# Performance work log

Hardware: AMD Instinct MI355X
Metric: run time of the kernel (lower is better)

The kernel has to match this reference:

```python
import jax, jax.numpy as jnp
import numpy as np

TEMPERATURE = 0.5
NUM_NEG_CANDIDATES = 8
HARD_NEG_K = 3


def setup_inputs() -> dict:
    key = jax.random.key(0)
    k1, k2 = jax.random.split(key)
    features = jax.random.normal(k1, (8192, 512), dtype=jnp.float32)
    labels = jax.random.randint(k2, (8192,), 0, 64, dtype=jnp.int64)
    return {"features": features, "labels": labels}


def reference(features, labels):
    B = features.shape[0]
    labels = labels.reshape(-1)
    # L2-normalize rows (torch F.normalize, eps=1e-12)
    f = features / jnp.maximum(jnp.linalg.norm(features, axis=1, keepdims=True), 1e-12)

    same = labels[:, None] == labels[None, :]          # [B, B]
    eye = jnp.eye(B, dtype=bool)
    neg_inf = jnp.float32(-jnp.inf)

    # Deterministic replacement for torch's randint/randperm sampling:
    # Gumbel-max = uniform sampling of one positive; Gumbel-top-m = sampling
    # m negatives without replacement.
    kp, kn = jax.random.split(jax.random.key(42))
    g_pos = jax.random.gumbel(kp, (B, B), dtype=jnp.float32)
    g_neg = jax.random.gumbel(kn, (B, B), dtype=jnp.float32)

    pos_mask = same & ~eye
    pos_j = jnp.argmax(jnp.where(pos_mask, g_pos, neg_inf), axis=1)   # [B]

    _, neg_idx = jax.lax.top_k(jnp.where(~same, g_neg, neg_inf), NUM_NEG_CANDIDATES)  # [B, m]

    cand = f[neg_idx]                                  # [B, m, D]
    neg_sims = jnp.einsum('bd,bmd->bm', f, cand)       # [B, m]
    hard_sims, _ = jax.lax.top_k(neg_sims, HARD_NEG_K)  # [B, k] hardest negatives

    pos_logit = jnp.sum(f * f[pos_j], axis=1) / TEMPERATURE          # [B]
    logits = jnp.concatenate([pos_logit[:, None], hard_sims / TEMPERATURE], axis=1)  # [B, 1+k]
    # cross-entropy with target index 0
    loss = jax.nn.logsumexp(logits, axis=1) - logits[:, 0]
    return jnp.mean(loss)
```

## Files before the change

### kernel.cpp

```cpp
#include <hip/hip_runtime.h>
#include <hip/hip_bf16.h>
#include <stdint.h>

#define BB 8192
#define DD 512
#define NNEG 8
#define CAP 256

#define VTHI 4273471488u

__host__ __device__ __forceinline__ uint32_t rotl32(uint32_t x, int r) {
#if defined(__HIP_DEVICE_COMPILE__)
  return __builtin_amdgcn_alignbit(x, x, 32 - r);
#else
  return (x << r) | (x >> (32 - r));
#endif
}

#define TF_RND(x0, x1, R) { x0 += x1; x1 = rotl32(x1, R); x1 ^= x0; }

__host__ __device__ __forceinline__ void threefry2x32(uint32_t k0, uint32_t k1,
                                                      uint32_t x0, uint32_t x1,
                                                      uint32_t& o0, uint32_t& o1) {
  uint32_t ks2 = k0 ^ k1 ^ 0x1BD11BDAu;
  x0 += k0; x1 += k1;
  TF_RND(x0, x1, 13) TF_RND(x0, x1, 15) TF_RND(x0, x1, 26) TF_RND(x0, x1, 6)
  x0 += k1; x1 += ks2 + 1u;
  TF_RND(x0, x1, 17) TF_RND(x0, x1, 29) TF_RND(x0, x1, 16) TF_RND(x0, x1, 24)
  x0 += ks2; x1 += k0 + 2u;
  TF_RND(x0, x1, 13) TF_RND(x0, x1, 15) TF_RND(x0, x1, 26) TF_RND(x0, x1, 6)
  x0 += k0; x1 += k1 + 3u;
  TF_RND(x0, x1, 17) TF_RND(x0, x1, 29) TF_RND(x0, x1, 16) TF_RND(x0, x1, 24)
  x0 += k1; x1 += ks2 + 4u;
  TF_RND(x0, x1, 13) TF_RND(x0, x1, 15) TF_RND(x0, x1, 26) TF_RND(x0, x1, 6)
  x0 += ks2; x1 += k0 + 5u;
  o0 = x0; o1 = x1;
}

__device__ __forceinline__ void tf_uniform(uint32_t k0, uint32_t k1, uint32_t x1pk,
                                           uint32_t& o0, uint32_t& o1) {
  uint32_t ks2 = k0 ^ k1 ^ 0x1BD11BDAu;
  uint32_t x0 = k0, x1 = x1pk;
  TF_RND(x0, x1, 13) TF_RND(x0, x1, 15) TF_RND(x0, x1, 26) TF_RND(x0, x1, 6)
  x0 += k1; x1 += ks2 + 1u;
  TF_RND(x0, x1, 17) TF_RND(x0, x1, 29) TF_RND(x0, x1, 16) TF_RND(x0, x1, 24)
  x0 += ks2; x1 += k0 + 2u;
  TF_RND(x0, x1, 13) TF_RND(x0, x1, 15) TF_RND(x0, x1, 26) TF_RND(x0, x1, 6)
  x0 += k0; x1 += k1 + 3u;
  TF_RND(x0, x1, 17) TF_RND(x0, x1, 29) TF_RND(x0, x1, 16) TF_RND(x0, x1, 24)
  x0 += k1; x1 += ks2 + 4u;
  TF_RND(x0, x1, 13) TF_RND(x0, x1, 15) TF_RND(x0, x1, 26) TF_RND(x0, x1, 6)
  x0 += ks2; x1 += k0 + 5u;
  o0 = x0; o1 = x1;
}

#define RND4(R) { TF_RND(x0a, x1a, R) TF_RND(x0b, x1b, R) TF_RND(x0c, x1c, R) TF_RND(x0d, x1d, R) }
#define INJ4(A, B) { uint32_t _b = (B); \
  x0a += (A); x1a += _b; x0b += (A); x1b += _b; x0c += (A); x1c += _b; x0d += (A); x1d += _b; }

__device__ __forceinline__ void tf_uniform4(uint32_t k0, uint32_t k1, uint32_t ctr,
                                            uint32_t bits[4]) {
  uint32_t ks2 = k0 ^ k1 ^ 0x1BD11BDAu;
  uint32_t x0a = k0, x1a = ctr;
  uint32_t x0b = k0, x1b = ctr + 64u;
  uint32_t x0c = k0, x1c = ctr + 128u;
  uint32_t x0d = k0, x1d = ctr + 192u;
  RND4(13) RND4(15) RND4(26) RND4(6)
  INJ4(k1, ks2 + 1u)
  RND4(17) RND4(29) RND4(16) RND4(24)
  INJ4(ks2, k0 + 2u)
  RND4(13) RND4(15) RND4(26) RND4(6)
  INJ4(k0, k1 + 3u)
  RND4(17) RND4(29) RND4(16) RND4(24)
  INJ4(k1, ks2 + 4u)
  RND4(13) RND4(15) RND4(26) RND4(6)
  INJ4(ks2, k0 + 5u)
  bits[0] = x0a ^ x1a; bits[1] = x0b ^ x1b; bits[2] = x0c ^ x1c; bits[3] = x0d ^ x1d;
}

__device__ __forceinline__ unsigned long long u64max(unsigned long long a, unsigned long long b) {
  return a > b ? a : b;
}
#define CE_DESC(m, x, y) { if (m[x] < m[y]) { unsigned long long _t = m[x]; m[x] = m[y]; m[y] = _t; } }
#define TOP8_INSERT(top, key) \
  if ((key) > top[7]) { \
    top[7] = (key); \
    _Pragma("unroll") \
    for (int s = 7; s > 0; --s) { \
      if (top[s] > top[s - 1]) { \
        unsigned long long _tt = top[s - 1]; top[s - 1] = top[s]; top[s] = _tt; \
      } \
    } \
  }

__device__ __forceinline__ void wave_merge_top8(unsigned long long top[8]) {
  #pragma unroll
  for (int d = 1; d < 64; d <<= 1) {
    unsigned long long o[8];
    #pragma unroll
    for (int r = 0; r < 8; ++r) o[r] = __shfl_xor(top[r], d, 64);
    unsigned long long m[8];
    #pragma unroll
    for (int r = 0; r < 8; ++r) m[r] = u64max(top[r], o[7 - r]);
    CE_DESC(m, 0, 4) CE_DESC(m, 1, 5) CE_DESC(m, 2, 6) CE_DESC(m, 3, 7)
    CE_DESC(m, 0, 2) CE_DESC(m, 1, 3) CE_DESC(m, 4, 6) CE_DESC(m, 5, 7)
    CE_DESC(m, 0, 1) CE_DESC(m, 2, 3) CE_DESC(m, 4, 5) CE_DESC(m, 6, 7)
    #pragma unroll
    for (int r = 0; r < 8; ++r) top[r] = m[r];
  }
}

__global__ __launch_bounds__(256) void prep_kernel(const float* __restrict__ feat,
                                                   const int* __restrict__ labels,
                                                   float* __restrict__ inv_norm,
                                                   uint16_t* __restrict__ lists,
                                                   int* __restrict__ offs) {
  if (blockIdx.x == 0) {
    __shared__ uint32_t hist[64];
    __shared__ uint32_t base[64];
    int t = threadIdx.x;
    if (t < 64) hist[t] = 0u;
    __syncthreads();
    for (int e = t; e < BB; e += 256) atomicAdd(&hist[labels[e] & 63], 1u);
    __syncthreads();
    if (t == 0) {
      uint32_t s = 0;
      for (int l = 0; l < 64; ++l) { base[l] = s; offs[l] = (int)s; s += hist[l]; }
      offs[64] = (int)s;
    }
    __syncthreads();
    for (int e = t; e < BB; e += 256) {
      uint32_t p = atomicAdd(&base[labels[e] & 63], 1u);
      lists[p] = (uint16_t)e;
    }
  } else {
    int wave = threadIdx.x >> 6, lane = threadIdx.x & 63;
    int row = (blockIdx.x - 1) * 4 + wave;
    const float4* fr = (const float4*)(feat + (size_t)row * DD);
    float4 a = fr[lane], b = fr[lane + 64];
    float s = a.x * a.x + a.y * a.y + a.z * a.z + a.w * a.w
            + b.x * b.x + b.y * b.y + b.z * b.z + b.w * b.w;
    #pragma unroll
    for (int d = 1; d < 64; d <<= 1) s += __shfl_xor(s, d, 64);
    if (lane == 0) inv_norm[row] = 1.0f / fmaxf(sqrtf(s), 1e-12f);
  }
}

__global__ __launch_bounds__(256) void scan_kernel(const int* __restrict__ labels,
                                                   const uint16_t* __restrict__ lists,
                                                   const int* __restrict__ offs,
                                                   uint32_t kp0, uint32_t kp1,
                                                   uint32_t kn0, uint32_t kn1,
                                                   int* __restrict__ pos_j,
                                                   int* __restrict__ neg_idx) {
  __shared__ uint2 buf[4][CAP];
  int wave = threadIdx.x >> 6, lane = threadIdx.x & 63;
  int i = blockIdx.x * 4 + wave;
  int li = labels[i];
  uint32_t rowbase = (uint32_t)i * (uint32_t)BB;
  uint32_t count = 0;

  uint32_t cb = rowbase + kn1 + (uint32_t)lane;
  for (int it = 0; it < BB / 256; ++it) {
    uint32_t bits[4];
    tf_uniform4(kn0, kn1, cb + (uint32_t)(it * 256), bits);
    #pragma unroll
    for (int c = 0; c < 4; ++c) {
      bool cand = bits[c] >= VTHI;
      unsigned long long m = __ballot(cand);
      if (m) {
        if (cand) {
          int ofs = __builtin_amdgcn_mbcnt_hi((uint32_t)(m >> 32),
                     __builtin_amdgcn_mbcnt_lo((uint32_t)m, 0));
          uint32_t p = count + (uint32_t)ofs;
          if (p < CAP) {
            uint2 e; e.x = bits[c]; e.y = (uint32_t)(it * 256 + c * 64 + lane);
            buf[wave][p] = e;
          }
        }
        count += (uint32_t)__popcll(m);
      }
    }
  }

  unsigned long long best = 0ull;
  int beg = offs[li], end = offs[li + 1];
  for (int t = beg + lane; t < end; t += 64) {
    int j = lists[t];
    if (j != i) {
      uint32_t o0, o1;
      tf_uniform(kp0, kp1, rowbase + kp1 + (uint32_t)j, o0, o1);
      unsigned long long key =
          (((unsigned long long)((o0 ^ o1) >> 9) << 13) | (unsigned)(8191 - j)) + 1ull;
      best = u64max(best, key);
    }
  }
  #pragma unroll
  for (int d = 1; d < 64; d <<= 1) best = u64max(best, __shfl_xor(best, d, 64));

  unsigned long long top[8] = {0ull,0ull,0ull,0ull,0ull,0ull,0ull,0ull};
  if (count <= CAP) {
    for (int t = lane; t < (int)count; t += 64) {
      uint2 e = buf[wave][t];
      uint32_t j = e.y;
      if (labels[j] != li) {
        unsigned long long key =
            (((unsigned long long)(e.x >> 9) << 13) | (unsigned)(8191u - j)) + 1ull;
        TOP8_INSERT(top, key)
      }
    }
  } else {
    for (int j = lane; j < BB; j += 64) {
      if (labels[j] != li) {
        uint32_t o0, o1;
        tf_uniform(kn0, kn1, rowbase + kn1 + (uint32_t)j, o0, o1);
        unsigned long long key =
            (((unsigned long long)((o0 ^ o1) >> 9) << 13) | (unsigned)(8191 - j)) + 1ull;
        TOP8_INSERT(top, key)
      }
    }
  }
  wave_merge_top8(top);

  uint32_t hi = VTHI;
  while (top[7] == 0ull && hi != 0u) {
    unsigned long long W = 0x100000000ull - (unsigned long long)hi;
    uint32_t newhi = (W * 8ull >= 0x100000000ull) ? 0u
                     : (uint32_t)(0x100000000ull - W * 8ull);
    for (int j = lane; j < BB; j += 64) {
      if (labels[j] != li) {
        uint32_t o0, o1;
        tf_uniform(kn0, kn1, rowbase + kn1 + (uint32_t)j, o0, o1);
        uint32_t bits = o0 ^ o1;
        if (bits >= newhi && bits < hi) {
          unsigned long long key =
              (((unsigned long long)(bits >> 9) << 13) | (unsigned)(8191 - j)) + 1ull;
          TOP8_INSERT(top, key)
        }
      }
    }
    wave_merge_top8(top);
    hi = newhi;
  }

  if (lane == 0) {
    pos_j[i] = best ? (8191 - (int)((best - 1ull) & 0x1FFFull)) : 0;
    #pragma unroll
    for (int r = 0; r < NNEG; ++r)
      neg_idx[i * 8 + r] = top[r] ? (8191 - (int)((top[r] - 1ull) & 0x1FFFull)) : r;
  }
}

__global__ __launch_bounds__(256) void loss_kernel(const float* __restrict__ feat,
                                                   const float* __restrict__ inv_norm,
                                                   const int* __restrict__ pos_j,
                                                   const int* __restrict__ neg_idx,
                                                   float* __restrict__ out) {
  __shared__ float part[4];
  int wave = threadIdx.x >> 6, lane = threadIdx.x & 63;
  int i = blockIdx.x * 4 + wave;
  const float4* fi = (const float4*)(feat + (size_t)i * DD);
  float4 a0 = fi[lane], a1 = fi[lane + 64];

  int cand[9];
  cand[0] = pos_j[i];
  #pragma unroll
  for (int m = 0; m < NNEG; ++m) cand[m + 1] = neg_idx[i * 8 + m];

  float4 c0[9], c1[9];
  #pragma unroll
  for (int c = 0; c < 9; ++c) {
    const float4* fc = (const float4*)(feat + (size_t)cand[c] * DD);
    c0[c] = fc[lane];
    c1[c] = fc[lane + 64];
  }
  float dots[9];
  #pragma unroll
  for (int c = 0; c < 9; ++c) {
    float s;
    s = a0.x * c0[c].x;
    s = fmaf(a0.y, c0[c].y, s); s = fmaf(a0.z, c0[c].z, s); s = fmaf(a0.w, c0[c].w, s);
    s = fmaf(a1.x, c1[c].x, s); s = fmaf(a1.y, c1[c].y, s);
    s = fmaf(a1.z, c1[c].z, s); s = fmaf(a1.w, c1[c].w, s);
    dots[c] = s;
  }
  #pragma unroll
  for (int c = 0; c < 9; ++c) {
    #pragma unroll
    for (int d = 1; d < 64; d <<= 1) dots[c] += __shfl_xor(dots[c], d, 64);
  }

  if (lane == 0) {
    float inv_i = inv_norm[i];
    float pos = dots[0] * inv_i * inv_norm[cand[0]] * 2.0f;
    float t1 = -1e30f, t2 = -1e30f, t3 = -1e30f;
    #pragma unroll
    for (int m = 0; m < NNEG; ++m) {
      float v = dots[m + 1] * inv_i * inv_norm[cand[m + 1]] * 2.0f;
      if (v > t1)      { t3 = t2; t2 = t1; t1 = v; }
      else if (v > t2) { t3 = t2; t2 = v; }
      else if (v > t3) { t3 = v; }
    }
    float mx = fmaxf(fmaxf(pos, t1), fmaxf(t2, t3));
    float lse = mx + logf(__expf(pos - mx) + __expf(t1 - mx) + __expf(t2 - mx) + __expf(t3 - mx));
    part[wave] = (lse - pos) * (1.0f / (float)BB);
  }
  __syncthreads();
  if (threadIdx.x == 0) atomicAdd(out, part[0] + part[1] + part[2] + part[3]);
}

extern "C" void kernel_launch(void* const* d_in, const int* in_sizes, int n_in,
                              void* d_out, int out_size, void* d_ws, size_t ws_size,
                              hipStream_t stream) {
  const float* features = (const float*)d_in[0];
  const int* labels = (const int*)d_in[1];
  float* out = (float*)d_out;

  char* w = (char*)d_ws;
  float* inv_norm = (float*)w;                    w += BB * sizeof(float);
  uint16_t* lists = (uint16_t*)w;                 w += BB * sizeof(uint16_t);
  int* offs = (int*)w;                            w += 65 * sizeof(int) + 28;
  int* pos_j = (int*)w;                           w += BB * sizeof(int);
  int* neg_idx = (int*)w;

  uint32_t kp0, kp1, kn0, kn1;
  threefry2x32(0u, 42u, 0u, 0u, kp0, kp1);
  threefry2x32(0u, 42u, 0u, 1u, kn0, kn1);

  hipMemsetAsync(d_out, 0, sizeof(float), stream);
  prep_kernel<<<BB / 4 + 1, 256, 0, stream>>>(features, labels, inv_norm, lists, offs);
  scan_kernel<<<BB / 4, 256, 0, stream>>>(labels, lists, offs, kp0, kp1, kn0, kn1,
                                          pos_j, neg_idx);
  loss_kernel<<<BB / 4, 256, 0, stream>>>(features, inv_norm, pos_j, neg_idx, out);
}
```

Before: 292.8 us.

## Fuse scan and loss kernels, compute norms inline, parallelize label bucketing

```diff
diff --git a/kernel.cpp b/kernel.cpp
--- a/kernel.cpp
+++ b/kernel.cpp
@@ -1,11 +1,11 @@
 #include <hip/hip_runtime.h>
-#include <hip/hip_bf16.h>
 #include <stdint.h>
 
 #define BB 8192
 #define DD 512
 #define NNEG 8
 #define CAP 256
+#define LSTRIDE 512
 
 #define VTHI 4273471488u
 
@@ -55,8 +55,12 @@
 }
 
 #define RND4(R) { TF_RND(x0a, x1a, R) TF_RND(x0b, x1b, R) TF_RND(x0c, x1c, R) TF_RND(x0d, x1d, R) }
-#define INJ4(A, B) { uint32_t _b = (B); \
-  x0a += (A); x1a += _b; x0b += (A); x1b += _b; x0c += (A); x1c += _b; x0d += (A); x1d += _b; }
+#define RND4_F(R, A) { \
+  x0a = x0a + (A) + x1a; x1a = rotl32(x1a, R); x1a ^= x0a; \
+  x0b = x0b + (A) + x1b; x1b = rotl32(x1b, R); x1b ^= x0b; \
+  x0c = x0c + (A) + x1c; x1c = rotl32(x1c, R); x1c ^= x0c; \
+  x0d = x0d + (A) + x1d; x1d = rotl32(x1d, R); x1d ^= x0d; }
+#define INJX1_4(B) { uint32_t _b = (B); x1a += _b; x1b += _b; x1c += _b; x1d += _b; }
 
 __device__ __forceinline__ void tf_uniform4(uint32_t k0, uint32_t k1, uint32_t ctr,
                                             uint32_t bits[4]) {
@@ -66,16 +70,19 @@
   uint32_t x0c = k0, x1c = ctr + 128u;
   uint32_t x0d = k0, x1d = ctr + 192u;
   RND4(13) RND4(15) RND4(26) RND4(6)
-  INJ4(k1, ks2 + 1u)
-  RND4(17) RND4(29) RND4(16) RND4(24)
-  INJ4(ks2, k0 + 2u)
-  RND4(13) RND4(15) RND4(26) RND4(6)
-  INJ4(k0, k1 + 3u)
-  RND4(17) RND4(29) RND4(16) RND4(24)
-  INJ4(k1, ks2 + 4u)
-  RND4(13) RND4(15) RND4(26) RND4(6)
-  INJ4(ks2, k0 + 5u)
-  bits[0] = x0a ^ x1a; bits[1] = x0b ^ x1b; bits[2] = x0c ^ x1c; bits[3] = x0d ^ x1d;
+  INJX1_4(ks2 + 1u)
+  RND4_F(17, k1) RND4(29) RND4(16) RND4(24)
+  INJX1_4(k0 + 2u)
+  RND4_F(13, ks2) RND4(15) RND4(26) RND4(6)
+  INJX1_4(k1 + 3u)
+  RND4_F(17, k0) RND4(29) RND4(16) RND4(24)
+  INJX1_4(ks2 + 4u)
+  RND4_F(13, k1) RND4(15) RND4(26) RND4(6)
+  uint32_t c5 = k0 + 5u;
+  bits[0] = (x0a + ks2) ^ (x1a + c5);
+  bits[1] = (x0b + ks2) ^ (x1b + c5);
+  bits[2] = (x0c + ks2) ^ (x1c + c5);
+  bits[3] = (x0d + ks2) ^ (x1d + c5);
 }
 
 __device__ __forceinline__ unsigned long long u64max(unsigned long long a, unsigned long long b) {
@@ -110,50 +117,32 @@
   }
 }
 
-__global__ __launch_bounds__(256) void prep_kernel(const float* __restrict__ feat,
+__global__ __launch_bounds__(256) void prep_kernel(const int* __restrict__ labels,
+                                                   uint16_t* __restrict__ lists,
+                                                   int* __restrict__ cnts) {
+  __shared__ uint32_t c;
+  int l = blockIdx.x;
+  if (threadIdx.x == 0) c = 0u;
+  __syncthreads();
+  for (int t = threadIdx.x; t < BB; t += 256) {
+    if (labels[t] == l) {
+      uint32_t p = atomicAdd(&c, 1u);
+      if (p < LSTRIDE) lists[l * LSTRIDE + p] = (uint16_t)t;
+    }
+  }
+  __syncthreads();
+  if (threadIdx.x == 0) cnts[l] = (int)c;
+}
+
+__global__ __launch_bounds__(256) void main_kernel(const float* __restrict__ feat,
                                                    const int* __restrict__ labels,
-                                                   float* __restrict__ inv_norm,
-                                                   uint16_t* __restrict__ lists,
-                                                   int* __restrict__ offs) {
-  if (blockIdx.x == 0) {
-    __shared__ uint32_t hist[64];
-    __shared__ uint32_t base[64];
-    int t = threadIdx.x;
-    if (t < 64) hist[t] = 0u;
-    __syncthreads();
-    for (int e = t; e < BB; e += 256) atomicAdd(&hist[labels[e] & 63], 1u);
-    __syncthreads();
-    if (t == 0) {
-      uint32_t s = 0;
-      for (int l = 0; l < 64; ++l) { base[l] = s; offs[l] = (int)s; s += hist[l]; }
-      offs[64] = (int)s;
-    }
-    __syncthreads();
-    for (int e = t; e < BB; e += 256) {
-      uint32_t p = atomicAdd(&base[labels[e] & 63], 1u);
-      lists[p] = (uint16_t)e;
-    }
-  } else {
-    int wave = threadIdx.x >> 6, lane = threadIdx.x & 63;
-    int row = (blockIdx.x - 1) * 4 + wave;
-    const float4* fr = (const float4*)(feat + (size_t)row * DD);
-    float4 a = fr[lane], b = fr[lane + 64];
-    float s = a.x * a.x + a.y * a.y + a.z * a.z + a.w * a.w
-            + b.x * b.x + b.y * b.y + b.z * b.z + b.w * b.w;
-    #pragma unroll
-    for (int d = 1; d < 64; d <<= 1) s += __shfl_xor(s, d, 64);
-    if (lane == 0) inv_norm[row] = 1.0f / fmaxf(sqrtf(s), 1e-12f);
-  }
-}
-
-__global__ __launch_bounds__(256) void scan_kernel(const int* __restrict__ labels,
                                                    const uint16_t* __restrict__ lists,
-                                                   const int* __restrict__ offs,
+                                                   const int* __restrict__ cnts,
                                                    uint32_t kp0, uint32_t kp1,
                                                    uint32_t kn0, uint32_t kn1,
-                                                   int* __restrict__ pos_j,
-                                                   int* __restrict__ neg_idx) {
+                                                   float* __restrict__ out) {
   __shared__ uint2 buf[4][CAP];
+  __shared__ float part[4];
   int wave = threadIdx.x >> 6, lane = threadIdx.x & 63;
   int i = blockIdx.x * 4 + wave;
   int li = labels[i];
@@ -184,15 +173,28 @@
   }
 
   unsigned long long best = 0ull;
-  int beg = offs[li], end = offs[li + 1];
-  for (int t = beg + lane; t < end; t += 64) {
-    int j = lists[t];
-    if (j != i) {
-      uint32_t o0, o1;
-      tf_uniform(kp0, kp1, rowbase + kp1 + (uint32_t)j, o0, o1);
-      unsigned long long key =
-          (((unsigned long long)((o0 ^ o1) >> 9) << 13) | (unsigned)(8191 - j)) + 1ull;
-      best = u64max(best, key);
+  int lc = cnts[li];
+  if (lc <= LSTRIDE) {
+    const uint16_t* seg = lists + li * LSTRIDE;
+    for (int t = lane; t < lc; t += 64) {
+      int j = seg[t];
+      if (j != i) {
+        uint32_t o0, o1;
+        tf_uniform(kp0, kp1, rowbase + kp1 + (uint32_t)j, o0, o1);
+        unsigned long long key =
+            (((unsigned long long)((o0 ^ o1) >> 9) << 13) | (unsigned)(8191 - j)) + 1ull;
+        best = u64max(best, key);
+      }
+    }
+  } else {
+    for (int j = lane; j < BB; j += 64) {
+      if (labels[j] == li && j != i) {
+        uint32_t o0, o1;
+        tf_uniform(kp0, kp1, rowbase + kp1 + (uint32_t)j, o0, o1);
+        unsigned long long key =
+            (((unsigned long long)((o0 ^ o1) >> 9) << 13) | (unsigned)(8191 - j)) + 1ull;
+        best = u64max(best, key);
+      }
     }
   }
   #pragma unroll
@@ -243,60 +245,54 @@
     hi = newhi;
   }
 
-  if (lane == 0) {
-    pos_j[i] = best ? (8191 - (int)((best - 1ull) & 0x1FFFull)) : 0;
-    #pragma unroll
-    for (int r = 0; r < NNEG; ++r)
-      neg_idx[i * 8 + r] = top[r] ? (8191 - (int)((top[r] - 1ull) & 0x1FFFull)) : r;
-  }
-}
-
-__global__ __launch_bounds__(256) void loss_kernel(const float* __restrict__ feat,
-                                                   const float* __restrict__ inv_norm,
-                                                   const int* __restrict__ pos_j,
-                                                   const int* __restrict__ neg_idx,
-                                                   float* __restrict__ out) {
-  __shared__ float part[4];
-  int wave = threadIdx.x >> 6, lane = threadIdx.x & 63;
-  int i = blockIdx.x * 4 + wave;
+  int cand[9];
+  cand[0] = best ? (8191 - (int)((best - 1ull) & 0x1FFFull)) : 0;
+  #pragma unroll
+  for (int r = 0; r < NNEG; ++r)
+    cand[r + 1] = top[r] ? (8191 - (int)((top[r] - 1ull) & 0x1FFFull)) : r;
+
   const float4* fi = (const float4*)(feat + (size_t)i * DD);
   float4 a0 = fi[lane], a1 = fi[lane + 64];
-
-  int cand[9];
-  cand[0] = pos_j[i];
-  #pragma unroll
-  for (int m = 0; m < NNEG; ++m) cand[m + 1] = neg_idx[i * 8 + m];
-
-  float4 c0[9], c1[9];
+  float sii = a0.x * a0.x + a0.y * a0.y + a0.z * a0.z + a0.w * a0.w
+            + a1.x * a1.x + a1.y * a1.y + a1.z * a1.z + a1.w * a1.w;
+  float dots[9], selfs[9];
   #pragma unroll
   for (int c = 0; c < 9; ++c) {
     const float4* fc = (const float4*)(feat + (size_t)cand[c] * DD);
-    c0[c] = fc[lane];
-    c1[c] = fc[lane + 64];
-  }
-  float dots[9];
-  #pragma unroll
-  for (int c = 0; c < 9; ++c) {
+    float4 c0 = fc[lane], c1 = fc[lane + 64];
     float s;
-    s = a0.x * c0[c].x;
-    s = fmaf(a0.y, c0[c].y, s); s = fmaf(a0.z, c0[c].z, s); s = fmaf(a0.w, c0[c].w, s);
-    s = fmaf(a1.x, c1[c].x, s); s = fmaf(a1.y, c1[c].y, s);
-    s = fmaf(a1.z, c1[c].z, s); s = fmaf(a1.w, c1[c].w, s);
+    s = a0.x * c0.x;
+    s = fmaf(a0.y, c0.y, s); s = fmaf(a0.z, c0.z, s); s = fmaf(a0.w, c0.w, s);
+    s = fmaf(a1.x, c1.x, s); s = fmaf(a1.y, c1.y, s);
+    s = fmaf(a1.z, c1.z, s); s = fmaf(a1.w, c1.w, s);
     dots[c] = s;
-  }
-  #pragma unroll
-  for (int c = 0; c < 9; ++c) {
-    #pragma unroll
-    for (int d = 1; d < 64; d <<= 1) dots[c] += __shfl_xor(dots[c], d, 64);
+    float q;
+    q = c0.x * c0.x;
+    q = fmaf(c0.y, c0.y, q); q = fmaf(c0.z, c0.z, q); q = fmaf(c0.w, c0.w, q);
+    q = fmaf(c1.x, c1.x, q); q = fmaf(c1.y, c1.y, q);
+    q = fmaf(c1.z, c1.z, q); q = fmaf(c1.w, c1.w, q);
+    selfs[c] = q;
+  }
+  #pragma unroll
+  for (int d = 1; d < 64; d <<= 1) {
+    sii += __shfl_xor(sii, d, 64);
+    #pragma unroll
+    for (int c = 0; c < 9; ++c) {
+      dots[c] += __shfl_xor(dots[c], d, 64);
+      selfs[c] += __shfl_xor(selfs[c], d, 64);
+    }
   }
 
   if (lane == 0) {
-    float inv_i = inv_norm[i];
-    float pos = dots[0] * inv_i * inv_norm[cand[0]] * 2.0f;
+    float inv_i = 1.0f / fmaxf(sqrtf(sii), 1e-12f);
+    float inv_c[9];
+    #pragma unroll
+    for (int c = 0; c < 9; ++c) inv_c[c] = 1.0f / fmaxf(sqrtf(selfs[c]), 1e-12f);
+    float pos = dots[0] * inv_i * inv_c[0] * 2.0f;
     float t1 = -1e30f, t2 = -1e30f, t3 = -1e30f;
     #pragma unroll
     for (int m = 0; m < NNEG; ++m) {
-      float v = dots[m + 1] * inv_i * inv_norm[cand[m + 1]] * 2.0f;
+      float v = dots[m + 1] * inv_i * inv_c[m + 1] * 2.0f;
       if (v > t1)      { t3 = t2; t2 = t1; t1 = v; }
       else if (v > t2) { t3 = t2; t2 = v; }
       else if (v > t3) { t3 = v; }
@@ -316,20 +312,15 @@
   const int* labels = (const int*)d_in[1];
   float* out = (float*)d_out;
 
-  char* w = (char*)d_ws;
-  float* inv_norm = (float*)w;                    w += BB * sizeof(float);
-  uint16_t* lists = (uint16_t*)w;                 w += BB * sizeof(uint16_t);
-  int* offs = (int*)w;                            w += 65 * sizeof(int) + 28;
-  int* pos_j = (int*)w;                           w += BB * sizeof(int);
-  int* neg_idx = (int*)w;
+  uint16_t* lists = (uint16_t*)d_ws;
+  int* cnts = (int*)((char*)d_ws + 64 * LSTRIDE * sizeof(uint16_t));
 
   uint32_t kp0, kp1, kn0, kn1;
   threefry2x32(0u, 42u, 0u, 0u, kp0, kp1);
   threefry2x32(0u, 42u, 0u, 1u, kn0, kn1);
 
   hipMemsetAsync(d_out, 0, sizeof(float), stream);
-  prep_kernel<<<BB / 4 + 1, 256, 0, stream>>>(features, labels, inv_norm, lists, offs);
-  scan_kernel<<<BB / 4, 256, 0, stream>>>(labels, lists, offs, kp0, kp1, kn0, kn1,
-                                          pos_j, neg_idx);
-  loss_kernel<<<BB / 4, 256, 0, stream>>>(features, inv_norm, pos_j, neg_idx, out);
-}
+  prep_kernel<<<64, 256, 0, stream>>>(labels, lists, cnts);
+  main_kernel<<<BB / 4, 256, 0, stream>>>(features, labels, lists, cnts,
+                                          kp0, kp1, kn0, kn1, out);
+}
```

After: 251.0 us. 14.3% less time.
